# Optimization experiments

Measured on AMD Instinct MI355X. Metric: run time of the kernel, lower is better.

Reference implementation:

```python
import jax, jax.numpy as jnp
import numpy as np

N_QUBITS = 12
N_LAYERS = 4
DIM = 2 ** N_QUBITS  # 4096
BATCH = 8192


def _cnot_perm(control: int, target: int) -> np.ndarray:
    """Permutation for CNOT: flip target bit where control bit is 1."""
    idx = np.arange(DIM)
    ctrl = (idx >> control) & 1
    return np.where(ctrl == 1, idx ^ (1 << target), idx)


# Compose the cyclic CNOT ring q0->q1->...->q(n-1)->q0 into one permutation.
_RING = np.arange(DIM)
for _i in range(N_QUBITS):
    _RING = _RING[_cnot_perm(_i, (_i + 1) % N_QUBITS)]
RING_PERM = _RING

# Pauli-Z sign table: SIGNS[q, i] = +1 if bit q of i is 0 else -1.
_bits = (np.arange(DIM)[None, :] >> np.arange(N_QUBITS)[:, None]) & 1
SIGNS = (1 - 2 * _bits).astype(np.float32)  # (n_qubits, DIM)


def _apply_ry(sr, si, angle, q):
    """Apply RY(angle) on qubit q. State kept as (real, imag) float arrays (B, DIM).
    RY has real matrix [[c, -s], [s, c]] so real/imag parts transform independently."""
    B = sr.shape[0]
    hi = DIM >> (q + 1)
    lo = 1 << q
    c = jnp.cos(angle * 0.5)[:, None, None]
    s = jnp.sin(angle * 0.5)[:, None, None]

    def rot(a):
        a = a.reshape(B, hi, 2, lo)  # axis 2 is the value of bit q
        a0, a1 = a[:, :, 0, :], a[:, :, 1, :]
        return jnp.stack([c * a0 - s * a1, s * a0 + c * a1], axis=2).reshape(B, DIM)

    return rot(sr), rot(si)


def setup_inputs() -> dict:
    key = jax.random.key(0)
    kx, kt = jax.random.split(key)
    x = jax.random.normal(kx, (BATCH, N_QUBITS), dtype=jnp.float32)
    theta = jax.random.normal(kt, (N_LAYERS, N_QUBITS), dtype=jnp.float32) * 0.1
    return {"x": x, "theta": theta}


def reference(x, theta):
    B = x.shape[0]
    # |0...0> state
    sr = jnp.zeros((B, DIM), dtype=x.dtype).at[:, 0].set(1.0)
    si = jnp.zeros((B, DIM), dtype=x.dtype)
    # angle encoding: RY(x_i) on qubit i
    for q in range(N_QUBITS):
        sr, si = _apply_ry(sr, si, x[:, q], q)
    ring = jnp.asarray(RING_PERM)
    for layer in range(N_LAYERS):
        for q in range(N_QUBITS):
            ang = jnp.broadcast_to(theta[layer, q], (B,))
            sr, si = _apply_ry(sr, si, ang, q)
        # cyclic CNOT entanglement (precomposed permutation)
        sr = sr[:, ring]
        si = si[:, ring]
    probs = sr * sr + si * si  # (B, DIM)
    return jnp.einsum("bd,qd->bq", probs, jnp.asarray(SIGNS))
```

## Files before the change

kernel.cpp:

```cpp
#include <hip/hip_runtime.h>

#define NQ    12
#define BATCH 8192

typedef float v2f __attribute__((ext_vector_type(2)));


constexpr int sig6(int x)            { return (x ^ (x << 1)) & 63; }
constexpr int sigpow6(int x, int t)  { return t == 0 ? x : sigpow6(sig6(x), t - 1); }
constexpr int rowmask6(int j, int t) {
    int tt = (8 - (t % 8)) % 8;
    int m = 0;
    for (int i = 0; i < 6; ++i)
        if ((sigpow6(1 << i, tt) >> j) & 1) m |= 1 << i;
    return m;
}
constexpr bool par6(int x) { return (__builtin_popcount(x & 63) & 1) != 0; }

#define VAT(w, i) w[(i) >> 1][(i) & 1]

template<int C>
__device__ __forceinline__ float dppf(float x) {
    return __int_as_float(__builtin_amdgcn_mov_dpp(__float_as_int(x), C, 0xF, 0xF, true));
}

template<int M>
__device__ __forceinline__ float shx(float x) {
    static_assert(M > 0 && M < 64, "mask");
    constexpr int lo = M & 31;
    float y = x;
    if constexpr (lo == 1)       y = dppf<0xB1>(y);
    else if constexpr (lo == 2)  y = dppf<0x4E>(y);
    else if constexpr (lo == 3)  y = dppf<0x1B>(y);
    else if constexpr (lo == 7)  y = dppf<0x141>(y);
    else if constexpr (lo == 15) y = dppf<0x140>(y);
    else if constexpr (lo != 0)
        y = __int_as_float(__builtin_amdgcn_ds_swizzle(__float_as_int(y),
                                                       0x1F | (lo << 10)));
    if constexpr ((M & 32) != 0) {
        int yi = __float_as_int(y);
        auto p = __builtin_amdgcn_permlane32_swap(yi, yi, false, false);
        y = (__int_as_float(p[0]) + __int_as_float(p[1])) - y;
    }
    return y;
}

template<int M>
__device__ __forceinline__ float wave_red(float x) {
    { float o = dppf<0xB1>(x); x = (M & 1)  ? x - o : x + o; }
    { float o = dppf<0x4E>(x); x = (M & 2)  ? x - o : x + o; }
    { float o = __int_as_float(__builtin_amdgcn_ds_swizzle(__float_as_int(x), 0x1F | (4  << 10))); x = (M & 4)  ? x - o : x + o; }
    { float o = __int_as_float(__builtin_amdgcn_ds_swizzle(__float_as_int(x), 0x1F | (8  << 10))); x = (M & 8)  ? x - o : x + o; }
    { float o = __int_as_float(__builtin_amdgcn_ds_swizzle(__float_as_int(x), 0x1F | (16 << 10))); x = (M & 16) ? x - o : x + o; }
    int xi = __float_as_int(x);
    auto p = __builtin_amdgcn_permlane32_swap(xi, xi, false, false);
    float s = __int_as_float(p[0]) + __int_as_float(p[1]);
    return (M & 32) ? (2.0f * x - s) : s;
}

__device__ __forceinline__ float wave_prod(float x) {
    x *= dppf<0xB1>(x);
    x *= dppf<0x4E>(x);
    x *= __int_as_float(__builtin_amdgcn_ds_swizzle(__float_as_int(x), 0x1F | (4  << 10)));
    x *= __int_as_float(__builtin_amdgcn_ds_swizzle(__float_as_int(x), 0x1F | (8  << 10)));
    x *= __int_as_float(__builtin_amdgcn_ds_swizzle(__float_as_int(x), 0x1F | (16 << 10)));
    int xi = __float_as_int(x);
    auto p = __builtin_amdgcn_permlane32_swap(xi, xi, false, false);
    return __int_as_float(p[0]) * __int_as_float(p[1]);
}

__device__ __forceinline__ float rl(float v, int l) {
    return __int_as_float(__builtin_amdgcn_readlane(__float_as_int(v), l));
}

template<int T, int Q>
__device__ __forceinline__ void regRY(v2f* w, float t) {
    constexpr int D = sigpow6(1 << Q, T);
    const v2f tMM = {-t, -t}, tPP = {t, t}, tMP = {-t, t}, tPM = {t, -t};
    if constexpr (Q == 0) {
        constexpr int K = D >> 1;
        #pragma unroll
        for (int k = 0; k < 32; ++k) {
            const int k2 = k ^ K;
            if (k2 < k) continue;
            v2f a = w[k], b = w[k2];
            v2f sb = {b[1], b[0]}, sa = {a[1], a[0]};
            w[k]  = __builtin_elementwise_fma(tMP, sb, a);
            w[k2] = __builtin_elementwise_fma(tMP, sa, b);
        }
    } else {
        constexpr int K  = D >> 1;
        constexpr int RM = rowmask6(Q, T);
        #pragma unroll
        for (int k = 0; k < 32; ++k) {
            const int k2 = k ^ K;
            if (k2 < k) continue;
            const bool p = par6((2 * k) & RM);
            if constexpr (RM & 1) {
                v2f a = w[k], b = w[k2];
                const v2f tk  = p ? tPM : tMP;
                const v2f tk2 = p ? tMP : tPM;
                w[k]  = __builtin_elementwise_fma(tk,  b, a);
                w[k2] = __builtin_elementwise_fma(tk2, a, b);
            } else {
                if (p) {
                    v2f a = w[k2], b = w[k];
                    w[k2] = __builtin_elementwise_fma(tMM, b, a);
                    w[k]  = __builtin_elementwise_fma(tPP, a, b);
                } else {
                    v2f a = w[k], b = w[k2];
                    w[k]  = __builtin_elementwise_fma(tMM, b, a);
                    w[k2] = __builtin_elementwise_fma(tPP, a, b);
                }
            }
        }
    }
}

template<int T>
__device__ __forceinline__ void c56A(v2f* w) {
    constexpr int ML = sigpow6(1, T);
    #pragma unroll
    for (int r = 32; r < 64; ++r) {
        const int pr = sigpow6(r, T + 1);
        VAT(w, pr) = shx<ML>(VAT(w, pr));
    }
}
template<int T>
__device__ __forceinline__ void c110A(v2f* w, int lane) {
    const bool cond = par6(lane & rowmask6(5, T + 1));
    constexpr int D = sigpow6(1, T + 1);
    #pragma unroll
    for (int r0 = 0; r0 < 64; r0 += 2) {
        const int a0 = sigpow6(r0, T + 1);
        const int a1 = a0 ^ D;
        float x0 = VAT(w, a0), x1 = VAT(w, a1);
        VAT(w, a0) = cond ? x1 : x0;
        VAT(w, a1) = cond ? x0 : x1;
    }
}
template<int T>
__device__ __forceinline__ void c56B(v2f* w, int lane) {
    const bool cond = par6(lane & rowmask6(5, T + 1));
    constexpr int D = sigpow6(1, T);
    #pragma unroll
    for (int r0 = 0; r0 < 64; r0 += 2) {
        const int a0 = sigpow6(r0, T);
        const int a1 = a0 ^ D;
        float x0 = VAT(w, a0), x1 = VAT(w, a1);
        VAT(w, a0) = cond ? x1 : x0;
        VAT(w, a1) = cond ? x0 : x1;
    }
}
template<int T>
__device__ __forceinline__ void c110B(v2f* w) {
    constexpr int ML = sigpow6(1, T + 1);
    #pragma unroll
    for (int r = 32; r < 64; ++r) {
        const int pr = sigpow6(r, T + 1);
        VAT(w, pr) = shx<ML>(VAT(w, pr));
    }
}
template<int T>
__device__ __forceinline__ void ringA(v2f* w, int lane) { c56A<T>(w); c110A<T>(w, lane); }
template<int T>
__device__ __forceinline__ void ringB(v2f* w, int lane) { c56B<T>(w, lane); c110B<T>(w); }

__device__ __forceinline__ void transpose64(v2f* w, float* sh, int lane) {
    const int row = lane & 31;
    const int rm  = (lane >> 1) * 66 + (lane & 1);
    v2f nv[16];
    if (lane < 32) {
        #pragma unroll
        for (int k = 0; k < 32; ++k)
            *reinterpret_cast<v2f*>(sh + row * 2 + k * 66) = w[k];
    }
    asm volatile("" ::: "memory");
    #pragma unroll
    for (int k = 0; k < 16; ++k) {
        nv[k][0] = sh[rm + 4 * k];
        nv[k][1] = sh[rm + 4 * k + 2];
    }
    asm volatile("" ::: "memory");
    if (lane >= 32) {
        #pragma unroll
        for (int k = 0; k < 32; ++k)
            *reinterpret_cast<v2f*>(sh + row * 2 + k * 66) = w[k];
    }
    asm volatile("" ::: "memory");
    #pragma unroll
    for (int k = 0; k < 16; ++k) {
        w[16 + k][0] = sh[rm + 4 * k];
        w[16 + k][1] = sh[rm + 4 * k + 2];
    }
    #pragma unroll
    for (int k = 0; k < 16; ++k) w[k] = nv[k];
    asm volatile("" ::: "memory");
}

template<int T>
__device__ __forceinline__ void layerA(v2f* w, int lane, float* sh, float t_l) {
    regRY<T, 0>(w, rl(t_l, T * NQ + 0));
    regRY<T, 1>(w, rl(t_l, T * NQ + 1));
    regRY<T, 2>(w, rl(t_l, T * NQ + 2));
    regRY<T, 3>(w, rl(t_l, T * NQ + 3));
    regRY<T, 4>(w, rl(t_l, T * NQ + 4));
    regRY<T, 5>(w, rl(t_l, T * NQ + 5));
    transpose64(w, sh, lane);
    regRY<T, 0>(w, rl(t_l, T * NQ + 6));
    regRY<T, 1>(w, rl(t_l, T * NQ + 7));
    regRY<T, 2>(w, rl(t_l, T * NQ + 8));
    regRY<T, 3>(w, rl(t_l, T * NQ + 9));
    regRY<T, 4>(w, rl(t_l, T * NQ + 10));
    regRY<T, 5>(w, rl(t_l, T * NQ + 11));
    ringB<T>(w, lane);
}

template<int T>
__device__ __forceinline__ void layerB(v2f* w, int lane, float* sh, float t_l) {
    regRY<T, 0>(w, rl(t_l, T * NQ + 6));
    regRY<T, 1>(w, rl(t_l, T * NQ + 7));
    regRY<T, 2>(w, rl(t_l, T * NQ + 8));
    regRY<T, 3>(w, rl(t_l, T * NQ + 9));
    regRY<T, 4>(w, rl(t_l, T * NQ + 10));
    regRY<T, 5>(w, rl(t_l, T * NQ + 11));
    transpose64(w, sh, lane);
    regRY<T, 0>(w, rl(t_l, T * NQ + 0));
    regRY<T, 1>(w, rl(t_l, T * NQ + 1));
    regRY<T, 2>(w, rl(t_l, T * NQ + 2));
    regRY<T, 3>(w, rl(t_l, T * NQ + 3));
    regRY<T, 4>(w, rl(t_l, T * NQ + 4));
    regRY<T, 5>(w, rl(t_l, T * NQ + 5));
    ringA<T>(w, lane);
}

__global__ __launch_bounds__(256)
void qc_kernel(const float* __restrict__ x, const float* __restrict__ theta,
               float* __restrict__ out) {
    __shared__ float shbuf[4][2112];
    const int lane = threadIdx.x & 63;
    const int wid  = threadIdx.x >> 6;
    const int b = __builtin_amdgcn_readfirstlane((blockIdx.x << 2) + wid);
    float* sh = &shbuf[wid][0];

    const float th_l = theta[lane < 48 ? lane : 0];
    float s5, c5;
    __sincosf(0.5f * th_l, &s5, &c5);
    const float t_l = s5 * __builtin_amdgcn_rcpf(c5);
    const float G = wave_prod((lane >= 12 && lane < 48) ? c5 : 1.0f);

    alignas(16) v2f w[32];

    float L = 1.0f;
    #pragma unroll
    for (int q = 6; q < NQ; ++q) {
        float s, c;
        __sincosf(0.5f * (x[b * NQ + q] + rl(th_l, q)), &s, &c);
        L *= ((lane >> (q - 6)) & 1) ? s : c;
    }
    {
        float s, c;
        __sincosf(0.5f * (x[b * NQ + 0] + rl(th_l, 0)), &s, &c);
        w[0] = {L * c, L * s};
    }
    #pragma unroll
    for (int q = 1; q < 6; ++q) {
        float s, c;
        __sincosf(0.5f * (x[b * NQ + q] + rl(th_l, q)), &s, &c);
        const v2f vs = {s, s}, vc = {c, c};
        #pragma unroll
        for (int k = 0; k < (1 << (q - 1)); ++k) {
            w[k + (1 << (q - 1))] = w[k] * vs;
            w[k]                  = w[k] * vc;
        }
    }

    ringA<0>(w, lane);
    layerA<1>(w, lane, sh, t_l);
    layerB<2>(w, lane, sh, t_l);
    layerA<3>(w, lane, sh, t_l);

    #pragma unroll
    for (int k = 0; k < 32; ++k) w[k] = w[k] * w[k];

    v2f u1[16], c1[16];
    #pragma unroll
    for (int m = 0; m < 16; ++m) {
        u1[m] = w[2 * m] + w[2 * m + 1];
        c1[m] = w[2 * m] - w[2 * m + 1];
    }
    v2f u2[8], d2v = {0.f, 0.f};
    #pragma unroll
    for (int m = 0; m < 8; ++m) {
        u2[m] = u1[2 * m] + u1[2 * m + 1];
        d2v  += u1[2 * m] - u1[2 * m + 1];
    }
    v2f c2[8];
    #pragma unroll
    for (int m = 0; m < 8; ++m) c2[m] = c1[2 * m] + c1[2 * m + 1];
    v2f u3[4], d3v = {0.f, 0.f};
    #pragma unroll
    for (int m = 0; m < 4; ++m) {
        u3[m] = u2[2 * m] + u2[2 * m + 1];
        d3v  += u2[2 * m] - u2[2 * m + 1];
    }
    v2f c3[4];
    #pragma unroll
    for (int m = 0; m < 4; ++m) c3[m] = c2[2 * m] + c2[2 * m + 1];
    v2f u4[2], c4[2];
    u4[0] = u3[0] + u3[1]; u4[1] = u3[2] + u3[3];
    v2f d4v = (u3[0] - u3[1]) + (u3[2] - u3[3]);
    c4[0] = c3[0] + c3[1]; c4[1] = c3[2] + c3[3];
    v2f U  = u4[0] + u4[1];
    v2f cS = c4[0] + c4[1];
    v2f cD = c4[0] - c4[1];

    const float tot = U[0] + U[1];
    float Dq[6];
    Dq[0] = U[0] - U[1];
    Dq[1] = cS[0] + cS[1];
    Dq[2] = d2v[0] + d2v[1];
    Dq[3] = d3v[0] + d3v[1];
    Dq[4] = d4v[0] - d4v[1];
    Dq[5] = cD[0] + cD[1];

    float res[NQ];
    res[0] = wave_red<rowmask6(0, 4)>(tot);
    res[1] = wave_red<rowmask6(1, 4)>(tot);
    res[2] = wave_red<rowmask6(2, 4)>(tot);
    res[3] = wave_red<rowmask6(3, 4)>(tot);
    res[4] = wave_red<rowmask6(4, 4)>(tot);
    res[5] = wave_red<rowmask6(5, 4)>(tot);
    #pragma unroll
    for (int j = 0; j < 6; ++j) res[6 + j] = wave_red<0>(Dq[j]);

    float myres = res[0];
    #pragma unroll
    for (int q = 1; q < NQ; ++q) myres = (lane == q) ? res[q] : myres;
    myres *= G * G;
    if (lane < NQ) out[b * NQ + lane] = myres;
}

extern "C" void kernel_launch(void* const* d_in, const int* in_sizes, int n_in,
                              void* d_out, int out_size, void* d_ws, size_t ws_size,
                              hipStream_t stream) {
    const float* x     = (const float*)d_in[0];
    const float* theta = (const float*)d_in[1];
    float* out = (float*)d_out;
    dim3 grid(BATCH / 4), block(256);
    qc_kernel<<<grid, block, 0, stream>>>(x, theta, out);
}
```

Baseline: 44.62 us.

## Fold CNOT lane-conditional swap into transpose indexing and sign-flipped RY; force packed FMA

The lane-conditional swap (c110A) of the CNOT ring is removed. It is absorbed into the next layer: the following qubit-0 RY gets a per-lane sign-flipped angle, and the transpose reads from a lane-xored shared-memory address. This drops 64 per-lane selects per ring application but adds address selection in the transpose. RY updates are also forced to v_pk_fma_f32 via inline asm so the compiler cannot split them, though the asm may block scheduling freedom.

```diff
diff --git a/kernel.cpp b/kernel.cpp
--- a/kernel.cpp
+++ b/kernel.cpp
@@ -18,6 +18,12 @@
 constexpr bool par6(int x) { return (__builtin_popcount(x & 63) & 1) != 0; }
 
 #define VAT(w, i) w[(i) >> 1][(i) & 1]
+
+__device__ __forceinline__ v2f pkfma(v2f a, v2f b, v2f c) {
+    v2f d;
+    asm("v_pk_fma_f32 %0, %1, %2, %3" : "=&v"(d) : "v"(a), "v"(b), "v"(c));
+    return d;
+}
 
 template<int C>
 __device__ __forceinline__ float dppf(float x) {
@@ -84,9 +90,10 @@
             const int k2 = k ^ K;
             if (k2 < k) continue;
             v2f a = w[k], b = w[k2];
-            v2f sb = {b[1], b[0]}, sa = {a[1], a[0]};
-            w[k]  = __builtin_elementwise_fma(tMP, sb, a);
-            w[k2] = __builtin_elementwise_fma(tMP, sa, b);
+            v2f sb = __builtin_shufflevector(b, b, 1, 0);
+            v2f sa = __builtin_shufflevector(a, a, 1, 0);
+            w[k]  = pkfma(tMP, sb, a);
+            w[k2] = pkfma(tMP, sa, b);
         }
     } else {
         constexpr int K  = D >> 1;
@@ -100,17 +107,17 @@
                 v2f a = w[k], b = w[k2];
                 const v2f tk  = p ? tPM : tMP;
                 const v2f tk2 = p ? tMP : tPM;
-                w[k]  = __builtin_elementwise_fma(tk,  b, a);
-                w[k2] = __builtin_elementwise_fma(tk2, a, b);
+                w[k]  = pkfma(tk,  b, a);
+                w[k2] = pkfma(tk2, a, b);
             } else {
                 if (p) {
                     v2f a = w[k2], b = w[k];
-                    w[k2] = __builtin_elementwise_fma(tMM, b, a);
-                    w[k]  = __builtin_elementwise_fma(tPP, a, b);
+                    w[k2] = pkfma(tMM, b, a);
+                    w[k]  = pkfma(tPP, a, b);
                 } else {
                     v2f a = w[k], b = w[k2];
-                    w[k]  = __builtin_elementwise_fma(tMM, b, a);
-                    w[k2] = __builtin_elementwise_fma(tPP, a, b);
+                    w[k]  = pkfma(tMM, b, a);
+                    w[k2] = pkfma(tPP, a, b);
                 }
             }
         }
@@ -124,19 +131,6 @@
     for (int r = 32; r < 64; ++r) {
         const int pr = sigpow6(r, T + 1);
         VAT(w, pr) = shx<ML>(VAT(w, pr));
-    }
-}
-template<int T>
-__device__ __forceinline__ void c110A(v2f* w, int lane) {
-    const bool cond = par6(lane & rowmask6(5, T + 1));
-    constexpr int D = sigpow6(1, T + 1);
-    #pragma unroll
-    for (int r0 = 0; r0 < 64; r0 += 2) {
-        const int a0 = sigpow6(r0, T + 1);
-        const int a1 = a0 ^ D;
-        float x0 = VAT(w, a0), x1 = VAT(w, a1);
-        VAT(w, a0) = cond ? x1 : x0;
-        VAT(w, a1) = cond ? x0 : x1;
     }
 }
 template<int T>
@@ -162,13 +156,14 @@
     }
 }
 template<int T>
-__device__ __forceinline__ void ringA(v2f* w, int lane) { c56A<T>(w); c110A<T>(w, lane); }
-template<int T>
 __device__ __forceinline__ void ringB(v2f* w, int lane) { c56B<T>(w, lane); c110B<T>(w); }
 
+template<int RM, int DX>
 __device__ __forceinline__ void transpose64(v2f* w, float* sh, int lane) {
     const int row = lane & 31;
-    const int rm  = (lane >> 1) * 66 + (lane & 1);
+    const int rm0 = (lane >> 1) * 66 + (lane & 1);
+    const int lx  = lane ^ DX;
+    const int rm1 = (lx >> 1) * 66 + (lx & 1);
     v2f nv[16];
     if (lane < 32) {
         #pragma unroll
@@ -178,8 +173,13 @@
     asm volatile("" ::: "memory");
     #pragma unroll
     for (int k = 0; k < 16; ++k) {
-        nv[k][0] = sh[rm + 4 * k];
-        nv[k][1] = sh[rm + 4 * k + 2];
+        if constexpr (RM == 0) {
+            nv[k][0] = sh[rm0 + 4 * k];
+            nv[k][1] = sh[rm0 + 4 * k + 2];
+        } else {
+            nv[k][0] = sh[(par6((2 * k)     & RM) ? rm1 : rm0) + 4 * k];
+            nv[k][1] = sh[(par6((2 * k + 1) & RM) ? rm1 : rm0) + 4 * k + 2];
+        }
     }
     asm volatile("" ::: "memory");
     if (lane >= 32) {
@@ -190,8 +190,13 @@
     asm volatile("" ::: "memory");
     #pragma unroll
     for (int k = 0; k < 16; ++k) {
-        w[16 + k][0] = sh[rm + 4 * k];
-        w[16 + k][1] = sh[rm + 4 * k + 2];
+        if constexpr (RM == 0) {
+            w[16 + k][0] = sh[rm0 + 4 * k];
+            w[16 + k][1] = sh[rm0 + 4 * k + 2];
+        } else {
+            w[16 + k][0] = sh[(par6((32 + 2 * k)     & RM) ? rm1 : rm0) + 4 * k];
+            w[16 + k][1] = sh[(par6((32 + 2 * k + 1) & RM) ? rm1 : rm0) + 4 * k + 2];
+        }
     }
     #pragma unroll
     for (int k = 0; k < 16; ++k) w[k] = nv[k];
@@ -200,13 +205,17 @@
 
 template<int T>
 __device__ __forceinline__ void layerA(v2f* w, int lane, float* sh, float t_l) {
-    regRY<T, 0>(w, rl(t_l, T * NQ + 0));
+    constexpr int RMD = rowmask6(5, T);
+    constexpr int DXD = sigpow6(1, T);
+    const bool cnd = (__popc(lane & RMD) & 1) != 0;
+    float t0 = rl(t_l, T * NQ + 0);
+    regRY<T, 0>(w, cnd ? -t0 : t0);
     regRY<T, 1>(w, rl(t_l, T * NQ + 1));
     regRY<T, 2>(w, rl(t_l, T * NQ + 2));
     regRY<T, 3>(w, rl(t_l, T * NQ + 3));
     regRY<T, 4>(w, rl(t_l, T * NQ + 4));
     regRY<T, 5>(w, rl(t_l, T * NQ + 5));
-    transpose64(w, sh, lane);
+    transpose64<RMD, DXD>(w, sh, lane);
     regRY<T, 0>(w, rl(t_l, T * NQ + 6));
     regRY<T, 1>(w, rl(t_l, T * NQ + 7));
     regRY<T, 2>(w, rl(t_l, T * NQ + 8));
@@ -224,14 +233,14 @@
     regRY<T, 3>(w, rl(t_l, T * NQ + 9));
     regRY<T, 4>(w, rl(t_l, T * NQ + 10));
     regRY<T, 5>(w, rl(t_l, T * NQ + 11));
-    transpose64(w, sh, lane);
+    transpose64<0, 0>(w, sh, lane);
     regRY<T, 0>(w, rl(t_l, T * NQ + 0));
     regRY<T, 1>(w, rl(t_l, T * NQ + 1));
     regRY<T, 2>(w, rl(t_l, T * NQ + 2));
     regRY<T, 3>(w, rl(t_l, T * NQ + 3));
     regRY<T, 4>(w, rl(t_l, T * NQ + 4));
     regRY<T, 5>(w, rl(t_l, T * NQ + 5));
-    ringA<T>(w, lane);
+    c56A<T>(w);
 }
 
 __global__ __launch_bounds__(256)
@@ -275,7 +284,7 @@
         }
     }
 
-    ringA<0>(w, lane);
+    c56A<0>(w);
     layerA<1>(w, lane, sh, t_l);
     layerB<2>(w, lane, sh, t_l);
     layerA<3>(w, lane, sh, t_l);
```

Measured after the change: 45.99 us. 3.1% more time.
